# Kernel optimization log

Hardware: AMD Instinct MI355X
Metric: run time of the kernel (lower is better)

The kernel has to match this reference:

```python
import jax, jax.numpy as jnp
import numpy as np

N_NODES = 100000
N_EDGES = 1600000
IN_CH = 128
OUT_CH = 128


def setup_inputs() -> dict:
    key = jax.random.key(0)
    k1, k2, k3 = jax.random.split(key, 3)
    x = jax.random.normal(k1, (N_NODES, IN_CH), dtype=jnp.float32)
    edge_index = jax.random.randint(k2, (2, N_EDGES), 0, N_NODES, dtype=jnp.int64)
    # glorot-like init for the linear weight, stored as [in, out]
    W = jax.random.normal(k3, (IN_CH, OUT_CH), dtype=jnp.float32) * (2.0 / (IN_CH + OUT_CH)) ** 0.5
    bias = jnp.zeros((OUT_CH,), dtype=jnp.float32)
    return {"x": x, "edge_index": edge_index, "W": W, "bias": bias}


def reference(x, edge_index, W, bias):
    N = x.shape[0]
    # linear transform (bias-free, matches Linear(in, out, bias=False))
    h = x @ W  # [N, out]

    # add self loops (improved=False -> fill_value = 1.0)
    loop = jnp.arange(N, dtype=edge_index.dtype)
    src = jnp.concatenate([edge_index[0], loop])
    dst = jnp.concatenate([edge_index[1], loop])
    ew = jnp.ones(src.shape[0], dtype=h.dtype)  # edge_weight None -> ones

    # symmetric GCN normalization: deg from dst, norm = d^-1/2[src] * w * d^-1/2[dst]
    deg = jax.ops.segment_sum(ew, dst, num_segments=N)
    deg_inv_sqrt = jnp.where(deg > 0, jax.lax.rsqrt(deg), 0.0)
    w = deg_inv_sqrt[src] * ew * deg_inv_sqrt[dst]

    # spmm aggregation: out[dst] += w * h[src]
    out = jax.ops.segment_sum(h[src] * w[:, None], dst, num_segments=N)
    return out + bias
```

## Files before the change

### kernel.cpp

```cpp
#include <hip/hip_runtime.h>
#include <hip/hip_bf16.h>

constexpr int kNodes = 100000;
constexpr int kEdges = 1600000;
constexpr int kCh    = 128;
constexpr int kCap   = 32;
constexpr int kLOvf  = 256;
constexpr int kBinShift = 7;
constexpr int kBinSize  = 1 << kBinShift;
constexpr int kBins  = (kNodes + kBinSize - 1) >> kBinShift;
constexpr int kABlocks = 128;
constexpr int kChunkCap = 32;
constexpr int kSpillCap = 64;
constexpr int kGemmBlocks = (kNodes + 127) / 128;

typedef __attribute__((ext_vector_type(8))) short short8;
typedef __attribute__((ext_vector_type(4))) float floatx4;
typedef __attribute__((ext_vector_type(4))) int   intx4;
typedef __attribute__((ext_vector_type(2))) float floatx2;


__global__ __launch_bounds__(512) void k_fused(const float* __restrict__ x,
                                               const float* __restrict__ W,
                                               const int* __restrict__ srcArr,
                                               const int* __restrict__ dstArr,
                                               unsigned* __restrict__ segs,
                                               int* __restrict__ segCnt,
                                               int* __restrict__ spillCnt,
                                               int* __restrict__ spillD,
                                               int* __restrict__ spillS,
                                               __hip_bfloat16* __restrict__ hs) {
  if (blockIdx.x < kABlocks) {
    __shared__ int lcnt[kBins];
    __shared__ int lspilln;
    for (int i = threadIdx.x; i < kBins; i += 512) lcnt[i] = 0;
    if (threadIdx.x == 0) lspilln = 0;
    __syncthreads();
    const intx4* d4 = (const intx4*)dstArr;
    const intx4* s4 = (const intx4*)srcArr;
    unsigned* myseg = segs + (long)blockIdx.x * kBins * kChunkCap;
    for (int i = blockIdx.x * 512 + (int)threadIdx.x; i < kEdges / 4; i += kABlocks * 512) {
      intx4 dv = __builtin_nontemporal_load(d4 + i);
      intx4 sv = __builtin_nontemporal_load(s4 + i);
      #pragma unroll
      for (int k = 0; k < 4; k++) {
        int d = dv[k], s = sv[k];
        int bin = d >> kBinShift;
        int pos = atomicAdd(&lcnt[bin], 1);
        if (pos < kChunkCap) {
          myseg[(bin << 5) + pos] = ((unsigned)(d & (kBinSize - 1)) << 17) | (unsigned)s;
        } else {
          int o = atomicAdd(&lspilln, 1);
          if (o < kSpillCap) {
            spillD[blockIdx.x * kSpillCap + o] = d;
            spillS[blockIdx.x * kSpillCap + o] = s;
          }
        }
      }
    }
    __syncthreads();
    for (int i = threadIdx.x; i < kBins; i += 512) {
      int c = lcnt[i];
      segCnt[blockIdx.x * kBins + i] = c < kChunkCap ? c : kChunkCap;
    }
    if (threadIdx.x == 0) {
      int n = lspilln;
      spillCnt[blockIdx.x] = n < kSpillCap ? n : kSpillCap;
    }
    return;
  }

  __shared__ short8 Bf[2048];
  for (int e = threadIdx.x; e < 2048; e += 512) {
    int lane = e & 63, c = (e >> 6) & 3, tt = e >> 8;
    int quad = lane >> 4, mcol = lane & 15;
    short8 v;
    #pragma unroll
    for (int j = 0; j < 8; j++) {
      __hip_bfloat16 h = __float2bfloat16(W[(c * 32 + quad * 8 + j) * kCh + tt * 16 + mcol]);
      v[j] = *(short*)&h;
    }
    Bf[e] = v;
  }
  __syncthreads();

  int wave = threadIdx.x >> 6;
  int lane = threadIdx.x & 63;
  int quad = lane >> 4;
  int mcol = lane & 15;
  int gb = blockIdx.x - kABlocks;
  long rowBase = ((long)gb * 8 + wave) * 16;
  if (rowBase >= kNodes) return;

  long arow = rowBase + mcol;
  if (arow >= kNodes) arow = kNodes - 1;
  const float* xp = x + arow * kCh;
  short8 afrag[4];
  #pragma unroll
  for (int c = 0; c < 4; c++) {
    const floatx4* p = (const floatx4*)(xp + c * 32 + quad * 8);
    floatx4 v0 = __builtin_nontemporal_load(p);
    floatx4 v1 = __builtin_nontemporal_load(p + 1);
    #pragma unroll
    for (int j = 0; j < 4; j++) {
      __hip_bfloat16 h0 = __float2bfloat16(v0[j]);
      __hip_bfloat16 h1 = __float2bfloat16(v1[j]);
      afrag[c][j]     = *(short*)&h0;
      afrag[c][j + 4] = *(short*)&h1;
    }
  }

  #pragma unroll
  for (int t = 0; t < 8; t++) {
    floatx4 acc = {0.f, 0.f, 0.f, 0.f};
    #pragma unroll
    for (int c = 0; c < 4; c++) {
      short8 b = Bf[(t * 4 + c) * 64 + lane];
      acc = __builtin_amdgcn_mfma_f32_16x16x32_bf16(afrag[c], b, acc, 0, 0, 0);
    }
    #pragma unroll
    for (int i = 0; i < 4; i++) {
      long r = rowBase + quad * 4 + i;
      if (r < kNodes) {
        __hip_bfloat16 h = __float2bfloat16(acc[i]);
        __builtin_nontemporal_store(*(short*)&h, (short*)hs + r * kCh + t * 16 + mcol);
      }
    }
  }
}


__global__ __launch_bounds__(256) void k_dinv(const unsigned* __restrict__ segs,
                                              const int* __restrict__ segCnt,
                                              const int* __restrict__ spillCnt,
                                              const int* __restrict__ spillD,
                                              float* __restrict__ dinv) {
  __shared__ int lsn[kABlocks];
  __shared__ int lsp[kABlocks];
  __shared__ int hist[kBinSize];
  int bin = blockIdx.x;
  for (int i = threadIdx.x; i < kABlocks; i += 256) {
    lsn[i] = segCnt[i * kBins + bin];
    lsp[i] = spillCnt[i];
  }
  for (int i = threadIdx.x; i < kBinSize; i += 256) hist[i] = 0;
  __syncthreads();

  for (int slot = threadIdx.x; slot < kABlocks * kChunkCap; slot += 256) {
    int blk = slot >> 5, pos = slot & 31;
    if (pos < lsn[blk]) {
      unsigned e = segs[((long)blk * kBins + bin) * kChunkCap + pos];
      atomicAdd(&hist[e >> 17], 1);
    }
  }
  for (int i = threadIdx.x; i < kABlocks * kSpillCap; i += 256) {
    int blk = i >> 6, o = i & 63;
    if (o < lsp[blk]) {
      int d = spillD[blk * kSpillCap + o];
      if ((d >> kBinShift) == bin) atomicAdd(&hist[d & (kBinSize - 1)], 1);
    }
  }
  __syncthreads();
  int base = bin << kBinShift;
  for (int i = threadIdx.x; i < kBinSize; i += 256) {
    int node = base + i;
    if (node < kNodes) dinv[node] = rsqrtf((float)(hist[i] + 1));
  }
}


__global__ __launch_bounds__(512) void k_agg(const unsigned* __restrict__ segs,
                                             const int* __restrict__ segCnt,
                                             const int* __restrict__ spillCnt,
                                             const int* __restrict__ spillD,
                                             const int* __restrict__ spillS,
                                             const float* __restrict__ dinv,
                                             const __hip_bfloat16* __restrict__ hs,
                                             const float* __restrict__ bias,
                                             float* __restrict__ out) {
  __shared__ int lsn[kABlocks];
  __shared__ int lsp[kABlocks];
  __shared__ int lcnt[kBinSize];
  __shared__ __align__(16) int lbkt[kBinSize][kCap];
  __shared__ unsigned lovf[kLOvf];
  __shared__ int lovfn;

  int bin  = blockIdx.x;
  int base = bin << kBinShift;

  for (int i = threadIdx.x; i < kABlocks; i += 512) {
    lsn[i] = segCnt[i * kBins + bin];
    lsp[i] = spillCnt[i];
  }
  for (int i = threadIdx.x; i < kBinSize; i += 512) lcnt[i] = 0;
  if (threadIdx.x == 0) lovfn = 0;
  __syncthreads();

  for (int slot = threadIdx.x; slot < kABlocks * kChunkCap; slot += 512) {
    int blk = slot >> 5, pos = slot & 31;
    if (pos < lsn[blk]) {
      unsigned e = segs[((long)blk * kBins + bin) * kChunkCap + pos];
      int r = (int)(e >> 17);
      int p = atomicAdd(&lcnt[r], 1);
      if (p < kCap) lbkt[r][p] = (int)(e & 0x1ffff);
      else { int o = atomicAdd(&lovfn, 1); if (o < kLOvf) lovf[o] = ((unsigned)r << 17) | (e & 0x1ffff); }
    }
  }
  for (int i = threadIdx.x; i < kABlocks * kSpillCap; i += 512) {
    int blk = i >> 6, o = i & 63;
    if (o < lsp[blk]) {
      int d = spillD[blk * kSpillCap + o];
      if ((d >> kBinShift) == bin) {
        int r = d & (kBinSize - 1);
        int s = spillS[blk * kSpillCap + o];
        int p = atomicAdd(&lcnt[r], 1);
        if (p < kCap) lbkt[r][p] = s;
        else { int o2 = atomicAdd(&lovfn, 1); if (o2 < kLOvf) lovf[o2] = ((unsigned)r << 17) | (unsigned)s; }
      }
    }
  }
  __syncthreads();

  int wave = threadIdx.x >> 6;
  int lane = threadIdx.x & 63;
  const __hip_bfloat162* hbase = (const __hip_bfloat162*)hs;
  int novf = lovfn; if (novf > kLOvf) novf = kLOvf;

  for (int t = 0; t < 16; t++) {
    int r = wave * 16 + t;
    int node = base + r;
    if (node >= kNodes) continue;

    float dd = dinv[node];
    float2 sf = __bfloat1622float2(hbase[(long)node * (kCh / 2) + lane]);
    float acc0 = dd * sf.x;
    float acc1 = dd * sf.y;

    int c = lcnt[r]; if (c > kCap) c = kCap;
    int j = 0;
    for (; j + 7 < c; j += 8) {
      int s[8];
      #pragma unroll
      for (int u = 0; u < 8; u++) s[u] = lbkt[r][j + u];
      float dv[8];
      #pragma unroll
      for (int u = 0; u < 8; u++) dv[u] = dinv[s[u]];
      __hip_bfloat162 v[8];
      #pragma unroll
      for (int u = 0; u < 8; u++) v[u] = hbase[(long)s[u] * (kCh / 2) + lane];
      #pragma unroll
      for (int u = 0; u < 8; u++) {
        float2 f = __bfloat1622float2(v[u]);
        acc0 = fmaf(dv[u], f.x, acc0);
        acc1 = fmaf(dv[u], f.y, acc1);
      }
    }
    for (; j < c; ++j) {
      int s = lbkt[r][j];
      float dv = dinv[s];
      float2 f = __bfloat1622float2(hbase[(long)s * (kCh / 2) + lane]);
      acc0 = fmaf(dv, f.x, acc0);
      acc1 = fmaf(dv, f.y, acc1);
    }
    for (int i = 0; i < novf; i++) {
      if ((int)(lovf[i] >> 17) == r) {
        int s = (int)(lovf[i] & 0x1ffff);
        float2 f = __bfloat1622float2(hbase[(long)s * (kCh / 2) + lane]);
        acc0 = fmaf(dinv[s], f.x, acc0);
        acc1 = fmaf(dinv[s], f.y, acc1);
      }
    }

    float2 b = ((const float2*)bias)[lane];
    floatx2 o;
    o[0] = dd * acc0 + b.x;
    o[1] = dd * acc1 + b.y;
    __builtin_nontemporal_store(o, (floatx2*)(out + (long)node * kCh) + lane);
  }
}


extern "C" void kernel_launch(void* const* d_in, const int* in_sizes, int n_in,
                              void* d_out, int out_size, void* d_ws, size_t ws_size,
                              hipStream_t stream) {
  const float* x    = (const float*)d_in[0];
  const int*   ei   = (const int*)d_in[1];
  const float* W    = (const float*)d_in[2];
  const float* bias = (const float*)d_in[3];
  float* out = (float*)d_out;

  const int* srcArr = ei;
  const int* dstArr = ei + kEdges;

  char* ws = (char*)d_ws;
  size_t off = 0;
  __hip_bfloat16* hs = (__hip_bfloat16*)(ws + off); off += (size_t)kNodes * kCh * 2;
  unsigned* segs = (unsigned*)(ws + off); off += (size_t)kABlocks * kBins * kChunkCap * 4;
  float* dinv    = (float*)   (ws + off); off += (size_t)kNodes * 4;
  int*   segCnt  = (int*)     (ws + off); off += (size_t)kABlocks * kBins * 4;
  int*   spillCnt= (int*)     (ws + off); off += (size_t)kABlocks * 4;
  int*   spillD  = (int*)     (ws + off); off += (size_t)kABlocks * kSpillCap * 4;
  int*   spillS  = (int*)     (ws + off); off += (size_t)kABlocks * kSpillCap * 4;

  k_fused<<<kABlocks + kGemmBlocks, 512, 0, stream>>>(x, W, srcArr, dstArr,
                                                      segs, segCnt, spillCnt, spillD, spillS, hs);

  k_dinv<<<kBins, 256, 0, stream>>>(segs, segCnt, spillCnt, spillD, dinv);

  k_agg<<<kBins, 512, 0, stream>>>(segs, segCnt, spillCnt, spillD, spillS,
                                   dinv, hs, bias, out);
}
```

Before: 233.8 us.

## Fuse bucketing, GEMM, degree and aggregation into one cooperative kernel

```diff
diff --git a/kernel.cpp b/kernel.cpp
--- a/kernel.cpp
+++ b/kernel.cpp
@@ -1,5 +1,8 @@
 #include <hip/hip_runtime.h>
 #include <hip/hip_bf16.h>
+#include <hip/hip_cooperative_groups.h>
+
+namespace cg = cooperative_groups;
 
 constexpr int kNodes = 100000;
 constexpr int kEdges = 1600000;
@@ -13,11 +16,243 @@
 constexpr int kChunkCap = 32;
 constexpr int kSpillCap = 64;
 constexpr int kGemmBlocks = (kNodes + 127) / 128;
+constexpr int kMegaBlocks = kABlocks + kGemmBlocks;
 
 typedef __attribute__((ext_vector_type(8))) short short8;
 typedef __attribute__((ext_vector_type(4))) float floatx4;
 typedef __attribute__((ext_vector_type(4))) int   intx4;
 typedef __attribute__((ext_vector_type(2))) float floatx2;
+
+
+union SMem {
+  int lcntA[kBins];
+  short8 Bf[2048];
+  struct {
+    int lsn[kABlocks];
+    int lsp[kABlocks];
+    int lcnt[kBinSize];
+    int lbkt[kBinSize][kCap];
+    unsigned lovf[kLOvf];
+    int lovfn;
+  } agg;
+};
+
+__global__ __launch_bounds__(512, 8) void k_mega(const float* __restrict__ x,
+                                                 const float* __restrict__ W,
+                                                 const int* __restrict__ srcArr,
+                                                 const int* __restrict__ dstArr,
+                                                 unsigned* __restrict__ segs,
+                                                 int* __restrict__ segCnt,
+                                                 int* __restrict__ spillCnt,
+                                                 int* __restrict__ spillD,
+                                                 int* __restrict__ spillS,
+                                                 __hip_bfloat16* __restrict__ hs,
+                                                 float* __restrict__ dinv,
+                                                 const float* __restrict__ bias,
+                                                 float* __restrict__ out) {
+  cg::grid_group grid = cg::this_grid();
+  __shared__ SMem sm;
+  __shared__ int lspilln;
+
+  if (blockIdx.x < kABlocks) {
+    for (int i = threadIdx.x; i < kBins; i += 512) sm.lcntA[i] = 0;
+    if (threadIdx.x == 0) lspilln = 0;
+    __syncthreads();
+    const intx4* d4 = (const intx4*)dstArr;
+    const intx4* s4 = (const intx4*)srcArr;
+    unsigned* myseg = segs + (long)blockIdx.x * kBins * kChunkCap;
+    for (int i = blockIdx.x * 512 + (int)threadIdx.x; i < kEdges / 4; i += kABlocks * 512) {
+      intx4 dv = __builtin_nontemporal_load(d4 + i);
+      intx4 sv = __builtin_nontemporal_load(s4 + i);
+      #pragma unroll
+      for (int k = 0; k < 4; k++) {
+        int d = dv[k], s = sv[k];
+        int bin = d >> kBinShift;
+        int pos = atomicAdd(&sm.lcntA[bin], 1);
+        if (pos < kChunkCap) {
+          myseg[(bin << 5) + pos] = ((unsigned)(d & (kBinSize - 1)) << 17) | (unsigned)s;
+        } else {
+          int o = atomicAdd(&lspilln, 1);
+          if (o < kSpillCap) {
+            spillD[blockIdx.x * kSpillCap + o] = d;
+            spillS[blockIdx.x * kSpillCap + o] = s;
+          }
+        }
+      }
+    }
+    __syncthreads();
+    for (int i = threadIdx.x; i < kBins; i += 512) {
+      int c = sm.lcntA[i];
+      segCnt[blockIdx.x * kBins + i] = c < kChunkCap ? c : kChunkCap;
+    }
+    if (threadIdx.x == 0) {
+      int n = lspilln;
+      spillCnt[blockIdx.x] = n < kSpillCap ? n : kSpillCap;
+    }
+  } else {
+    for (int e = threadIdx.x; e < 2048; e += 512) {
+      int lane = e & 63, c = (e >> 6) & 3, tt = e >> 8;
+      int quad = lane >> 4, mcol = lane & 15;
+      short8 v;
+      #pragma unroll
+      for (int j = 0; j < 8; j++) {
+        __hip_bfloat16 h = __float2bfloat16(W[(c * 32 + quad * 8 + j) * kCh + tt * 16 + mcol]);
+        v[j] = *(short*)&h;
+      }
+      sm.Bf[e] = v;
+    }
+    __syncthreads();
+
+    int wave = threadIdx.x >> 6;
+    int lane = threadIdx.x & 63;
+    int quad = lane >> 4;
+    int mcol = lane & 15;
+    int gb = blockIdx.x - kABlocks;
+    long rowBase = ((long)gb * 8 + wave) * 16;
+    if (rowBase < kNodes) {
+      long arow = rowBase + mcol;
+      if (arow >= kNodes) arow = kNodes - 1;
+      const float* xp = x + arow * kCh;
+      short8 afrag[4];
+      #pragma unroll
+      for (int c = 0; c < 4; c++) {
+        const floatx4* p = (const floatx4*)(xp + c * 32 + quad * 8);
+        floatx4 v0 = __builtin_nontemporal_load(p);
+        floatx4 v1 = __builtin_nontemporal_load(p + 1);
+        #pragma unroll
+        for (int j = 0; j < 4; j++) {
+          __hip_bfloat16 h0 = __float2bfloat16(v0[j]);
+          __hip_bfloat16 h1 = __float2bfloat16(v1[j]);
+          afrag[c][j]     = *(short*)&h0;
+          afrag[c][j + 4] = *(short*)&h1;
+        }
+      }
+      #pragma unroll
+      for (int t = 0; t < 8; t++) {
+        floatx4 acc = {0.f, 0.f, 0.f, 0.f};
+        #pragma unroll
+        for (int c = 0; c < 4; c++) {
+          short8 b = sm.Bf[(t * 4 + c) * 64 + lane];
+          acc = __builtin_amdgcn_mfma_f32_16x16x32_bf16(afrag[c], b, acc, 0, 0, 0);
+        }
+        #pragma unroll
+        for (int i = 0; i < 4; i++) {
+          long r = rowBase + quad * 4 + i;
+          if (r < kNodes) {
+            __hip_bfloat16 h = __float2bfloat16(acc[i]);
+            __builtin_nontemporal_store(*(short*)&h, (short*)hs + r * kCh + t * 16 + mcol);
+          }
+        }
+      }
+    }
+  }
+
+  __threadfence();
+  grid.sync();
+
+  int bin  = blockIdx.x;
+  int base = bin << kBinShift;
+  if (bin < kBins) {
+    for (int i = threadIdx.x; i < kABlocks; i += 512) {
+      sm.agg.lsn[i] = segCnt[i * kBins + bin];
+      sm.agg.lsp[i] = spillCnt[i];
+    }
+    for (int i = threadIdx.x; i < kBinSize; i += 512) sm.agg.lcnt[i] = 0;
+    if (threadIdx.x == 0) sm.agg.lovfn = 0;
+    __syncthreads();
+
+    for (int slot = threadIdx.x; slot < kABlocks * kChunkCap; slot += 512) {
+      int blk = slot >> 5, pos = slot & 31;
+      if (pos < sm.agg.lsn[blk]) {
+        unsigned e = segs[((long)blk * kBins + bin) * kChunkCap + pos];
+        int r = (int)(e >> 17);
+        int p = atomicAdd(&sm.agg.lcnt[r], 1);
+        if (p < kCap) sm.agg.lbkt[r][p] = (int)(e & 0x1ffff);
+        else { int o = atomicAdd(&sm.agg.lovfn, 1); if (o < kLOvf) sm.agg.lovf[o] = ((unsigned)r << 17) | (e & 0x1ffff); }
+      }
+    }
+    for (int i = threadIdx.x; i < kABlocks * kSpillCap; i += 512) {
+      int blk = i >> 6, o = i & 63;
+      if (o < sm.agg.lsp[blk]) {
+        int d = spillD[blk * kSpillCap + o];
+        if ((d >> kBinShift) == bin) {
+          int r = d & (kBinSize - 1);
+          int s = spillS[blk * kSpillCap + o];
+          int p = atomicAdd(&sm.agg.lcnt[r], 1);
+          if (p < kCap) sm.agg.lbkt[r][p] = s;
+          else { int o2 = atomicAdd(&sm.agg.lovfn, 1); if (o2 < kLOvf) sm.agg.lovf[o2] = ((unsigned)r << 17) | (unsigned)s; }
+        }
+      }
+    }
+    __syncthreads();
+    for (int r = threadIdx.x; r < kBinSize; r += 512) {
+      int node = base + r;
+      if (node < kNodes) dinv[node] = rsqrtf((float)(sm.agg.lcnt[r] + 1));
+    }
+  }
+
+  __threadfence();
+  grid.sync();
+
+  if (bin < kBins) {
+    int wave = threadIdx.x >> 6;
+    int lane = threadIdx.x & 63;
+    const __hip_bfloat162* hbase = (const __hip_bfloat162*)hs;
+    int novf = sm.agg.lovfn; if (novf > kLOvf) novf = kLOvf;
+
+    for (int t = 0; t < 16; t++) {
+      int r = wave * 16 + t;
+      int node = base + r;
+      if (node >= kNodes) continue;
+
+      float dd = rsqrtf((float)(sm.agg.lcnt[r] + 1));
+      float2 sf = __bfloat1622float2(hbase[(long)node * (kCh / 2) + lane]);
+      float acc0 = dd * sf.x;
+      float acc1 = dd * sf.y;
+
+      int c = sm.agg.lcnt[r]; if (c > kCap) c = kCap;
+      int j = 0;
+      for (; j + 7 < c; j += 8) {
+        int s[8];
+        #pragma unroll
+        for (int u = 0; u < 8; u++) s[u] = sm.agg.lbkt[r][j + u];
+        float dv[8];
+        #pragma unroll
+        for (int u = 0; u < 8; u++) dv[u] = dinv[s[u]];
+        __hip_bfloat162 v[8];
+        #pragma unroll
+        for (int u = 0; u < 8; u++) v[u] = hbase[(long)s[u] * (kCh / 2) + lane];
+        #pragma unroll
+        for (int u = 0; u < 8; u++) {
+          float2 f = __bfloat1622float2(v[u]);
+          acc0 = fmaf(dv[u], f.x, acc0);
+          acc1 = fmaf(dv[u], f.y, acc1);
+        }
+      }
+      for (; j < c; ++j) {
+        int s = sm.agg.lbkt[r][j];
+        float dv = dinv[s];
+        float2 f = __bfloat1622float2(hbase[(long)s * (kCh / 2) + lane]);
+        acc0 = fmaf(dv, f.x, acc0);
+        acc1 = fmaf(dv, f.y, acc1);
+      }
+      for (int i = 0; i < novf; i++) {
+        if ((int)(sm.agg.lovf[i] >> 17) == r) {
+          int s = (int)(sm.agg.lovf[i] & 0x1ffff);
+          float2 f = __bfloat1622float2(hbase[(long)s * (kCh / 2) + lane]);
+          acc0 = fmaf(dinv[s], f.x, acc0);
+          acc1 = fmaf(dinv[s], f.y, acc1);
+        }
+      }
+
+      float2 b = ((const float2*)bias)[lane];
+      floatx2 o;
+      o[0] = dd * acc0 + b.x;
+      o[1] = dd * acc1 + b.y;
+      __builtin_nontemporal_store(o, (floatx2*)(out + (long)node * kCh) + lane);
+    }
+  }
+}
 
 
 __global__ __launch_bounds__(512) void k_fused(const float* __restrict__ x,
@@ -109,7 +344,6 @@
       afrag[c][j + 4] = *(short*)&h1;
     }
   }
-
   #pragma unroll
   for (int t = 0; t < 8; t++) {
     floatx4 acc = {0.f, 0.f, 0.f, 0.f};
@@ -128,7 +362,6 @@
     }
   }
 }
-
 
 __global__ __launch_bounds__(256) void k_dinv(const unsigned* __restrict__ segs,
                                               const int* __restrict__ segCnt,
@@ -145,7 +378,6 @@
   }
   for (int i = threadIdx.x; i < kBinSize; i += 256) hist[i] = 0;
   __syncthreads();
-
   for (int slot = threadIdx.x; slot < kABlocks * kChunkCap; slot += 256) {
     int blk = slot >> 5, pos = slot & 31;
     if (pos < lsn[blk]) {
@@ -167,7 +399,6 @@
     if (node < kNodes) dinv[node] = rsqrtf((float)(hist[i] + 1));
   }
 }
-
 
 __global__ __launch_bounds__(512) void k_agg(const unsigned* __restrict__ segs,
                                              const int* __restrict__ segCnt,
@@ -302,11 +533,25 @@
   int*   spillD  = (int*)     (ws + off); off += (size_t)kABlocks * kSpillCap * 4;
   int*   spillS  = (int*)     (ws + off); off += (size_t)kABlocks * kSpillCap * 4;
 
+  int maxB = 0;
+  (void)hipOccupancyMaxActiveBlocksPerMultiprocessor(&maxB, (const void*)k_mega, 512, 0);
+  bool coop = (maxB * 256 >= kMegaBlocks);
+
+  if (coop) {
+    const float* x_ = x; const float* W_ = W;
+    const int* sA = srcArr; const int* dA = dstArr;
+    unsigned* sg = segs; int* sc = segCnt; int* spc = spillCnt; int* spd = spillD; int* sps = spillS;
+    __hip_bfloat16* hs_ = hs; float* dv_ = dinv; const float* b_ = bias; float* o_ = out;
+    void* args[] = {&x_, &W_, &sA, &dA, &sg, &sc, &spc, &spd, &sps, &hs_, &dv_, &b_, &o_};
+    hipError_t err = hipLaunchCooperativeKernel((const void*)k_mega,
+                                                dim3(kMegaBlocks), dim3(512),
+                                                args, 0, stream);
+    if (err == hipSuccess) return;
+  }
+
   k_fused<<<kABlocks + kGemmBlocks, 512, 0, stream>>>(x, W, srcArr, dstArr,
                                                       segs, segCnt, spillCnt, spillD, spillS, hs);
-
   k_dinv<<<kBins, 256, 0, stream>>>(segs, segCnt, spillCnt, spillD, dinv);
-
   k_agg<<<kBins, 512, 0, stream>>>(segs, segCnt, spillCnt, spillD, spillS,
                                    dinv, hs, bias, out);
 }
```

Result: no change. 234.0 us (+0.1%).
